# Performance work log

Hardware: AMD Instinct MI355X
Metric: run time of the kernel (lower is better)

The kernel has to match this reference:

```python
import jax, jax.numpy as jnp
import numpy as np

B, C, F = 4, 3, 51
H_OUT, W_OUT = 384, 384
H_IN, W_IN = H_OUT + F - 1, W_OUT + F - 1


def setup_inputs() -> dict:
    key = jax.random.key(0)
    k1, k2, k3 = jax.random.split(key, 3)
    tenIn = jax.random.normal(k1, (B, C, H_IN, W_IN), dtype=jnp.float32)
    tenVer = jax.random.uniform(k2, (B, F, H_OUT, W_OUT), dtype=jnp.float32)
    tenHor = jax.random.uniform(k3, (B, F, H_OUT, W_OUT), dtype=jnp.float32)
    return {"tenIn": tenIn, "tenVer": tenVer, "tenHor": tenHor}


def reference(tenIn, tenVer, tenHor):
    # Out[n,c,y,x] = sum_{fy,fx} In[n,c,y+fy,x+fx] * Ver[n,fy,y,x] * Hor[n,fx,y,x]
    b, c, h_in, w_in = tenIn.shape
    f = tenVer.shape[1]
    h_out, w_out = tenVer.shape[2], tenVer.shape[3]

    # Horizontal sliding windows of the input, built once (static slices):
    # wx[b,c,fx,y_in,x] = In[b,c,y_in,x+fx]  -> [B,C,F,H_in,W_out]
    wx = jnp.stack([tenIn[:, :, :, fx:fx + w_out] for fx in range(f)], axis=2)

    def step(acc, fy):
        # rows[b,c,fx,y,x] = In[b,c,y+fy,x+fx]  -> [B,C,F,H_out,W_out]
        rows = jax.lax.dynamic_slice_in_dim(wx, fy, h_out, axis=3)
        # horizontal contraction with per-pixel horizontal kernel
        a = jnp.einsum('bcfyx,bfyx->bcyx', rows, tenHor)
        # weight by per-pixel vertical kernel tap fy
        ver_fy = jax.lax.dynamic_slice_in_dim(tenVer, fy, 1, axis=1)  # [B,1,H,W]
        return acc + a * ver_fy, None

    out0 = jnp.zeros((b, c, h_out, w_out), dtype=tenIn.dtype)
    out, _ = jax.lax.scan(step, out0, jnp.arange(f))
    return out
```

## Files before the change

kernel.cpp:

```cpp
#include <hip/hip_runtime.h>

namespace {
constexpr int CC = 3, FF = 51;
constexpr int HOUT = 384, WOUT = 384;
constexpr int HIN = 434, WIN = 434;
constexpr int KY = 4;
constexpr int LANES = 64;
constexpr int NW = 4;
constexpr int EXT = LANES + FF - 1;
constexpr int LPAD = 128;
constexpr int NSTEP = FF + KY - 1;
constexpr int NSG = CC * LPAD / LANES;
constexpr int NQW = 4;
constexpr int NPW = 8;
constexpr int SSTRIDE = NW * CC * LPAD;

using half2v = _Float16 __attribute__((ext_vector_type(2)));

__device__ __forceinline__ float fdot2f(half2v a, half2v b, float c) {
#if __has_builtin(__builtin_amdgcn_fdot2)
  return __builtin_amdgcn_fdot2(a, b, c, false);
#else
  return c + (float)a.x * (float)b.x + (float)a.y * (float)b.y;
#endif
}
}

__global__ __launch_bounds__(NW* LANES, 2) void sepconv_kernel(
    const float* __restrict__ In, const float* __restrict__ Ver,
    const float* __restrict__ Hor, float* __restrict__ Out) {
  const int lane = threadIdx.x;
  const int w = threadIdx.y;
  const int x0 = blockIdx.x * LANES;
  const int y0 = blockIdx.y * KY;
  const int b = blockIdx.z;
  const int x = x0 + lane;
  const int fxBase = 13 * w;
  const int ntaps = (w < 3) ? 13 : 12;
  const int aw = (lane + fxBase) & 3;
  const int bw = lane + fxBase - aw;

  __shared__ __align__(16) unsigned short sIn[2][NW][CC][LPAD];
  __shared__ float sRed[NW - 1][CC][KY][LANES];
  unsigned short* const sflat = &sIn[0][0][0][0];

  const size_t HW = (size_t)HOUT * WOUT;

  half2v hp[KY][NPW];
  {
    const float* horx = Hor + (size_t)b * FF * HW + x;
#pragma unroll
    for (int t = 0; t < KY; ++t) {
      const float* hb = horx + (size_t)(y0 + t) * WOUT;
#pragma unroll
      for (int j = 0; j < NPW; ++j) {
        const int u0 = 2 * j - aw;
        const int u1 = u0 + 1;
        float f0 = (u0 >= 0 && u0 < ntaps) ? hb[(size_t)(fxBase + u0) * HW] : 0.0f;
        float f1 = (u1 >= 0 && u1 < ntaps) ? hb[(size_t)(fxBase + u1) * HW] : 0.0f;
        half2v p;
        p.x = (_Float16)f0;
        p.y = (_Float16)f1;
        hp[t][j] = p;
      }
    }
  }

  const float* inb = In + ((size_t)b * CC * HIN + y0) * WIN + x0;
  const float* verb = Ver + (size_t)b * FF * HW + (size_t)y0 * WOUT + x;

  float acc[CC][KY] = {};
  float sv[NSG];

#define STAGE_LOAD(R)                                                         \
  _Pragma("unroll") for (int k = 0; k < NSG; ++k) {                           \
    const int e = lane + (k & 1) * 64;                                        \
    const bool valid = ((k & 1) == 0) || (lane < EXT - LANES);                \
    sv[k] = valid ? inb[(size_t)((k >> 1) * HIN + (R)) * WIN + e] : 0.0f;     \
  }

#define STAGE_WRITE(BF)                                                       \
  _Pragma("unroll") for (int k = 0; k < NSG; ++k) {                           \
    const int e = lane + (k & 1) * 64;                                        \
    sflat[(BF)*SSTRIDE + (w * CC + (k >> 1)) * LPAD + e] =                    \
        __builtin_bit_cast(unsigned short, (_Float16)sv[k]);                  \
  }

#define COMPUTE(R, BF)                                                        \
  {                                                                           \
    float vv[KY];                                                             \
    _Pragma("unroll") for (int t = 0; t < KY; ++t) {                          \
      const int u = (R)-t;                                                    \
      vv[t] = (u >= 0 && u < FF)                                              \
                  ? verb[(size_t)u * HW + (size_t)t * WOUT]                   \
                  : 0.0f;                                                     \
    }                                                                         \
    _Pragma("unroll") for (int c = 0; c < CC; ++c) {                          \
      const unsigned short* rp = sflat + (BF)*SSTRIDE + (w * CC + c) * LPAD + bw; \
      float d[KY] = {};                                                       \
      _Pragma("unroll") for (int q = 0; q < NQW; ++q) {                       \
        const uint2 u2 = *reinterpret_cast<const uint2*>(rp + 4 * q);         \
        const half2v p0 = __builtin_bit_cast(half2v, u2.x);                   \
        const half2v p1 = __builtin_bit_cast(half2v, u2.y);                   \
        _Pragma("unroll") for (int t = 0; t < KY; ++t) {                      \
          d[t] = fdot2f(p0, hp[t][2 * q], d[t]);                              \
          d[t] = fdot2f(p1, hp[t][2 * q + 1], d[t]);                          \
        }                                                                     \
      }                                                                       \
      _Pragma("unroll") for (int t = 0; t < KY; ++t) acc[c][t] += d[t] * vv[t];\
    }                                                                         \
  }

  STAGE_LOAD(0);
  STAGE_WRITE(0);

#pragma unroll 1
  for (int r = 0; r < NSTEP; r += 2) {
    STAGE_LOAD(r + 1);
    COMPUTE(r, 0);
    STAGE_WRITE(1);
    const bool more = (r + 2 < NSTEP);
    if (more) { STAGE_LOAD(r + 2); }
    COMPUTE(r + 1, 1);
    if (more) { STAGE_WRITE(0); }
  }

  if (w > 0) {
#pragma unroll
    for (int c = 0; c < CC; ++c)
#pragma unroll
      for (int t = 0; t < KY; ++t) sRed[w - 1][c][t][lane] = acc[c][t];
  }
  __syncthreads();
  if (w == 0) {
    float* outb = Out + (size_t)b * CC * HW + (size_t)y0 * WOUT + x0 + lane;
#pragma unroll
    for (int c = 0; c < CC; ++c)
#pragma unroll
      for (int t = 0; t < KY; ++t)
        outb[(size_t)c * HW + (size_t)t * WOUT] =
            acc[c][t] + sRed[0][c][t][lane] + sRed[1][c][t][lane] +
            sRed[2][c][t][lane];
  }
#undef STAGE_LOAD
#undef STAGE_WRITE
#undef COMPUTE
}

extern "C" void kernel_launch(void* const* d_in, const int* in_sizes, int n_in,
                              void* d_out, int out_size, void* d_ws, size_t ws_size,
                              hipStream_t stream) {
  const float* In = (const float*)d_in[0];
  const float* Ver = (const float*)d_in[1];
  const float* Hor = (const float*)d_in[2];
  float* Out = (float*)d_out;

  dim3 grid(WOUT / LANES, HOUT / KY, 4);
  dim3 block(LANES, NW, 1);
  sepconv_kernel<<<grid, block, 0, stream>>>(In, Ver, Hor, Out);
}
```

Baseline: 163.9 us.

## Pre-convert input to fp16 and stream rows into LDS via global_load_lds

Adds a conversion kernel that writes the input image as fp16 into the workspace. The main kernel then streams each input row straight from global memory into LDS with the global_load_lds DMA builtin, instead of loading fp32 into registers, converting and storing to LDS. This removes per-row register staging and conversion work from the inner loop and frees VGPRs. The cost is an extra kernel launch and a full read/write pass over the input, plus reliance on correct waitcnt handling for the asynchronous LDS writes.

```diff
diff --git a/kernel.cpp b/kernel.cpp
--- a/kernel.cpp
+++ b/kernel.cpp
@@ -2,6 +2,7 @@
 
 namespace {
 constexpr int CC = 3, FF = 51;
+constexpr int BB = 4;
 constexpr int HOUT = 384, WOUT = 384;
 constexpr int HIN = 434, WIN = 434;
 constexpr int KY = 4;
@@ -14,6 +15,7 @@
 constexpr int NQW = 4;
 constexpr int NPW = 8;
 constexpr int SSTRIDE = NW * CC * LPAD;
+constexpr size_t IN16_BYTES = (size_t)BB * CC * HIN * WIN * 2;
 
 using half2v = _Float16 __attribute__((ext_vector_type(2)));
 
@@ -24,11 +26,30 @@
   return c + (float)a.x * (float)b.x + (float)a.y * (float)b.y;
 #endif
 }
-}
-
+
+#define GLLDS(G, L)                                                  \
+  __builtin_amdgcn_global_load_lds(                                  \
+      (const __attribute__((address_space(1))) void*)(G),            \
+      (__attribute__((address_space(3))) void*)(L), 4, 0, 0)
+}
+
+__global__ void cvt16_kernel(const float* __restrict__ in,
+                             unsigned int* __restrict__ out, int n2) {
+  int i = blockIdx.x * blockDim.x + threadIdx.x;
+  const int stride = gridDim.x * blockDim.x;
+  for (; i < n2; i += stride) {
+    const float2 v = *reinterpret_cast<const float2*>(in + 2 * (size_t)i);
+    const unsigned short lo = __builtin_bit_cast(unsigned short, (_Float16)v.x);
+    const unsigned short hi = __builtin_bit_cast(unsigned short, (_Float16)v.y);
+    out[i] = ((unsigned int)hi << 16) | lo;
+  }
+}
+
+template <bool DMA>
 __global__ __launch_bounds__(NW* LANES, 2) void sepconv_kernel(
     const float* __restrict__ In, const float* __restrict__ Ver,
-    const float* __restrict__ Hor, float* __restrict__ Out) {
+    const float* __restrict__ Hor, float* __restrict__ Out,
+    const unsigned short* __restrict__ In16) {
   const int lane = threadIdx.x;
   const int w = threadIdx.y;
   const int x0 = blockIdx.x * LANES;
@@ -68,6 +89,10 @@
 
   const float* inb = In + ((size_t)b * CC * HIN + y0) * WIN + x0;
   const float* verb = Ver + (size_t)b * FF * HW + (size_t)y0 * WOUT + x;
+  const unsigned short* in16b =
+      In16 + ((size_t)b * CC * HIN + y0) * WIN + x0;
+  const int vmax = 2 * WIN - 4 - 2 * x0;
+  const int voff = (4 * lane < vmax) ? 4 * lane : vmax;
 
   float acc[CC][KY] = {};
   float sv[NSG];
@@ -84,6 +109,12 @@
     const int e = lane + (k & 1) * 64;                                        \
     sflat[(BF)*SSTRIDE + (w * CC + (k >> 1)) * LPAD + e] =                    \
         __builtin_bit_cast(unsigned short, (_Float16)sv[k]);                  \
+  }
+
+#define STAGE_DMA(R, BF)                                                      \
+  _Pragma("unroll") for (int c = 0; c < CC; ++c) {                            \
+    const unsigned short* g = in16b + (size_t)(c * HIN + (R)) * WIN;          \
+    GLLDS((const char*)g + voff, &sIn[BF][w][c][0]);                          \
   }
 
 #define COMPUTE(R, BF)                                                        \
@@ -111,18 +142,27 @@
     }                                                                         \
   }
 
-  STAGE_LOAD(0);
-  STAGE_WRITE(0);
-
+  if constexpr (DMA) {
+    STAGE_DMA(0, 0);
+#pragma unroll 2
+    for (int r = 0; r < NSTEP; ++r) {
+      const int rn = (r + 1 < NSTEP) ? r + 1 : NSTEP - 1;
+      STAGE_DMA(rn, (r + 1) & 1);
+      COMPUTE(r, r & 1);
+    }
+  } else {
+    STAGE_LOAD(0);
+    STAGE_WRITE(0);
 #pragma unroll 1
-  for (int r = 0; r < NSTEP; r += 2) {
-    STAGE_LOAD(r + 1);
-    COMPUTE(r, 0);
-    STAGE_WRITE(1);
-    const bool more = (r + 2 < NSTEP);
-    if (more) { STAGE_LOAD(r + 2); }
-    COMPUTE(r + 1, 1);
-    if (more) { STAGE_WRITE(0); }
+    for (int r = 0; r < NSTEP; r += 2) {
+      STAGE_LOAD(r + 1);
+      COMPUTE(r, 0);
+      STAGE_WRITE(1);
+      const bool more = (r + 2 < NSTEP);
+      if (more) { STAGE_LOAD(r + 2); }
+      COMPUTE(r + 1, 1);
+      if (more) { STAGE_WRITE(0); }
+    }
   }
 
   if (w > 0) {
@@ -144,6 +184,7 @@
   }
 #undef STAGE_LOAD
 #undef STAGE_WRITE
+#undef STAGE_DMA
 #undef COMPUTE
 }
 
@@ -155,7 +196,16 @@
   const float* Hor = (const float*)d_in[2];
   float* Out = (float*)d_out;
 
-  dim3 grid(WOUT / LANES, HOUT / KY, 4);
+  dim3 grid(WOUT / LANES, HOUT / KY, BB);
   dim3 block(LANES, NW, 1);
-  sepconv_kernel<<<grid, block, 0, stream>>>(In, Ver, Hor, Out);
-}
+
+  if (ws_size >= IN16_BYTES && d_ws != nullptr) {
+    const int n2 = (int)(BB * CC * HIN * WIN / 2);
+    cvt16_kernel<<<2048, 256, 0, stream>>>(In, (unsigned int*)d_ws, n2);
+    sepconv_kernel<true><<<grid, block, 0, stream>>>(
+        In, Ver, Hor, Out, (const unsigned short*)d_ws);
+  } else {
+    sepconv_kernel<false><<<grid, block, 0, stream>>>(In, Ver, Hor, Out,
+                                                      nullptr);
+  }
+}
```

Measured after the change: 162.2 us. No clear change (-1.1%).

## Prefetch vertical weights one four-step group ahead and unroll the tap loop

Applied to the files above, without the earlier changes.

The vertical-kernel global loads move out of the per-step compute into double-buffered register arrays. Each array is filled four filter steps before it is used, and the main loop is unrolled by eight. Bounds checks are kept only in the prologue and epilogue, and the accumulation uses an explicit FMA. The goal is to hide global-memory latency on the Ver loads behind the fdot2 work, at the cost of 32 extra live registers per thread, which may reduce occupancy or cause spills.

```diff
diff --git a/kernel.cpp b/kernel.cpp
--- a/kernel.cpp
+++ b/kernel.cpp
@@ -2,6 +2,7 @@
 
 namespace {
 constexpr int CC = 3, FF = 51;
+constexpr int BB = 4;
 constexpr int HOUT = 384, WOUT = 384;
 constexpr int HIN = 434, WIN = 434;
 constexpr int KY = 4;
@@ -9,7 +10,6 @@
 constexpr int NW = 4;
 constexpr int EXT = LANES + FF - 1;
 constexpr int LPAD = 128;
-constexpr int NSTEP = FF + KY - 1;
 constexpr int NSG = CC * LPAD / LANES;
 constexpr int NQW = 4;
 constexpr int NPW = 8;
@@ -68,9 +68,14 @@
 
   const float* inb = In + ((size_t)b * CC * HIN + y0) * WIN + x0;
   const float* verb = Ver + (size_t)b * FF * HW + (size_t)y0 * WOUT + x;
+  const float* vbase0 = Ver + (size_t)b * FF * HW + (size_t)(y0 + 0) * WOUT + x0;
+  const float* vbase1 = Ver + (size_t)b * FF * HW + (size_t)(y0 + 1) * WOUT + x0;
+  const float* vbase2 = Ver + (size_t)b * FF * HW + (size_t)(y0 + 2) * WOUT + x0;
+  const float* vbase3 = Ver + (size_t)b * FF * HW + (size_t)(y0 + 3) * WOUT + x0;
 
   float acc[CC][KY] = {};
   float sv[NSG];
+  float vA[4 * KY], vB[4 * KY];
 
 #define STAGE_LOAD(R)                                                         \
   _Pragma("unroll") for (int k = 0; k < NSG; ++k) {                           \
@@ -86,19 +91,37 @@
         __builtin_bit_cast(unsigned short, (_Float16)sv[k]);                  \
   }
 
-#define COMPUTE(R, BF)                                                        \
+#define VV_S4(R, VS)                                                          \
+  _Pragma("unroll") for (int s = 0; s < 4; ++s) {                             \
+    VS[4 * s + 0] = vbase0[(size_t)((R) + s - 0) * HW + lane];                \
+    VS[4 * s + 1] = vbase1[(size_t)((R) + s - 1) * HW + lane];                \
+    VS[4 * s + 2] = vbase2[(size_t)((R) + s - 2) * HW + lane];                \
+    VS[4 * s + 3] = vbase3[(size_t)((R) + s - 3) * HW + lane];                \
+  }
+
+#define VV_G1(R, VS, S)                                                       \
+  _Pragma("unroll") for (int t = 0; t < KY; ++t) {                            \
+    const int u = (R)-t;                                                      \
+    VS[4 * (S) + t] = (u >= 0 && u < FF)                                      \
+                          ? verb[(size_t)u * HW + (size_t)t * WOUT]           \
+                          : 0.0f;                                             \
+  }
+
+#define COMPUTE(BF, VS, S)                                                    \
   {                                                                           \
-    float vv[KY];                                                             \
-    _Pragma("unroll") for (int t = 0; t < KY; ++t) {                          \
-      const int u = (R)-t;                                                    \
-      vv[t] = (u >= 0 && u < FF)                                              \
-                  ? verb[(size_t)u * HW + (size_t)t * WOUT]                   \
-                  : 0.0f;                                                     \
-    }                                                                         \
     _Pragma("unroll") for (int c = 0; c < CC; ++c) {                          \
       const unsigned short* rp = sflat + (BF)*SSTRIDE + (w * CC + c) * LPAD + bw; \
-      float d[KY] = {};                                                       \
-      _Pragma("unroll") for (int q = 0; q < NQW; ++q) {                       \
+      float d[KY];                                                            \
+      {                                                                       \
+        const uint2 u2 = *reinterpret_cast<const uint2*>(rp);                 \
+        const half2v p0 = __builtin_bit_cast(half2v, u2.x);                   \
+        const half2v p1 = __builtin_bit_cast(half2v, u2.y);                   \
+        _Pragma("unroll") for (int t = 0; t < KY; ++t) {                      \
+          d[t] = fdot2f(p0, hp[t][0], 0.0f);                                  \
+          d[t] = fdot2f(p1, hp[t][1], d[t]);                                  \
+        }                                                                     \
+      }                                                                       \
+      _Pragma("unroll") for (int q = 1; q < NQW; ++q) {                       \
         const uint2 u2 = *reinterpret_cast<const uint2*>(rp + 4 * q);         \
         const half2v p0 = __builtin_bit_cast(half2v, u2.x);                   \
         const half2v p1 = __builtin_bit_cast(half2v, u2.y);                   \
@@ -107,23 +130,39 @@
           d[t] = fdot2f(p1, hp[t][2 * q + 1], d[t]);                          \
         }                                                                     \
       }                                                                       \
-      _Pragma("unroll") for (int t = 0; t < KY; ++t) acc[c][t] += d[t] * vv[t];\
+      _Pragma("unroll") for (int t = 0; t < KY; ++t)                          \
+        acc[c][t] = __builtin_fmaf(d[t], VS[4 * (S) + t], acc[c][t]);         \
     }                                                                         \
   }
+
+#define STEP4(R, VS)                                                          \
+  STAGE_LOAD((R) + 1); COMPUTE(0, VS, 0); STAGE_WRITE(1);                     \
+  STAGE_LOAD((R) + 2); COMPUTE(1, VS, 1); STAGE_WRITE(0);                     \
+  STAGE_LOAD((R) + 3); COMPUTE(0, VS, 2); STAGE_WRITE(1);                     \
+  STAGE_LOAD((R) + 4); COMPUTE(1, VS, 3); STAGE_WRITE(0);
 
   STAGE_LOAD(0);
   STAGE_WRITE(0);
+  VV_G1(0, vA, 0); VV_G1(1, vA, 1); VV_G1(2, vA, 2); VV_G1(3, vA, 3);
+  VV_S4(4, vB);
+  STEP4(0, vA);
 
 #pragma unroll 1
-  for (int r = 0; r < NSTEP; r += 2) {
-    STAGE_LOAD(r + 1);
-    COMPUTE(r, 0);
-    STAGE_WRITE(1);
-    const bool more = (r + 2 < NSTEP);
-    if (more) { STAGE_LOAD(r + 2); }
-    COMPUTE(r + 1, 1);
-    if (more) { STAGE_WRITE(0); }
-  }
+  for (int r = 4; r < 44; r += 8) {
+    VV_S4(r + 4, vA);
+    STEP4(r, vB);
+    VV_S4(r + 8, vB);
+    STEP4(r + 4, vA);
+  }
+
+  VV_G1(48, vA, 0); VV_G1(49, vA, 1); VV_G1(50, vA, 2); VV_G1(51, vA, 3);
+  STEP4(44, vB);
+  VV_G1(52, vB, 0); VV_G1(53, vB, 1);
+  STEP4(48, vA);
+  STAGE_LOAD(53);
+  COMPUTE(0, vB, 0);
+  STAGE_WRITE(1);
+  COMPUTE(1, vB, 1);
 
   if (w > 0) {
 #pragma unroll
@@ -144,7 +183,10 @@
   }
 #undef STAGE_LOAD
 #undef STAGE_WRITE
+#undef VV_S4
+#undef VV_G1
 #undef COMPUTE
+#undef STEP4
 }
 
 extern "C" void kernel_launch(void* const* d_in, const int* in_sizes, int n_in,
@@ -155,7 +197,7 @@
   const float* Hor = (const float*)d_in[2];
   float* Out = (float*)d_out;
 
-  dim3 grid(WOUT / LANES, HOUT / KY, 4);
+  dim3 grid(WOUT / LANES, HOUT / KY, BB);
   dim3 block(LANES, NW, 1);
   sepconv_kernel<<<grid, block, 0, stream>>>(In, Ver, Hor, Out);
 }
```

Result: slower. 502.5 us (+206.6%).
